# Kernel tuning notes

Hardware: AMD Instinct MI355X
Metric: run time of the kernel (lower is better)

Reference implementation:

```python
import jax, jax.numpy as jnp
import numpy as np

# ---- constants lifted from EulerRNNCell / run_model ----
OMEGA_EPS = 1e-8          # inputs + 1e-08
GAMMA = 1.1               # self.params[1]
ETA = 0.36                # self.params[2]
DT = 2.0 ** (-8)          # deltat
MAXT = 1.0
NUM_TRAJ = 64
T = int(np.arange(0.0, MAXT, DT).shape[0])   # 256 time points
B = 512


def setup_inputs() -> dict:
    key = jax.random.key(0)
    k1, k2 = jax.random.split(key)
    inputs = jax.random.normal(k1, (B, 1), dtype=jnp.float32)      # per-sample Rabi rate Omega
    # rho0 = |0><0|  ->  Bloch vector (0, 0, 1)
    bloch0 = jnp.zeros((3,), dtype=jnp.float32).at[2].set(1.0)
    # unit normals; Euler-Maruyama scaling sqrt(DT) applied inside reference
    wvec = jax.random.normal(k2, (NUM_TRAJ * B, T - 1, 2), dtype=jnp.float32)
    return {"inputs": inputs, "bloch0": bloch0, "wvec": wvec}


def _euler_rollout(x0, omega, dw):
    """Sequential Euler-Maruyama rollout of the Genois qubit SDE.
    x0:    [N, 3]       initial Bloch vectors
    omega: [N]          per-trajectory Rabi rate (params[:,0])
    dw:    [T-1, N, 2]  Wiener increments (already scaled by sqrt(DT))
    returns x_T: [N, 3]
    """
    k = jnp.asarray(np.sqrt(GAMMA * ETA / 2.0), dtype=x0.dtype)  # measurement back-action strength

    def step(x, dwt):
        x1, x2, x3 = x[:, 0], x[:, 1], x[:, 2]
        # drift a(x, p): Rabi drive about x-axis + measurement dephasing at GAMMA/2
        ax = -0.5 * GAMMA * x1
        ay = -omega * x3 - 0.5 * GAMMA * x2
        az = omega * x2
        # diffusion b(x, p) @ dW: heterodyne sigma_z back-action (two quadratures)
        d1, d2 = dwt[:, 0], dwt[:, 1]
        bx = k * (-x1 * x3 * d1 + x2 * d2)
        by = k * (-x2 * x3 * d1 - x1 * d2)
        bz = k * ((1.0 - x3 * x3) * d1)
        xn = jnp.stack([x1 + DT * ax + bx,
                        x2 + DT * ay + by,
                        x3 + DT * az + bz], axis=1)
        return xn, None

    xT, _ = jax.lax.scan(step, x0, dw)
    return xT


def reference(inputs, bloch0, wvec):
    b = inputs.shape[0]
    n = NUM_TRAJ * b
    # traj_inputs = tile([inputs+eps, Gamma, eta], num_traj); only Omega varies per row
    omega = jnp.tile(inputs[:, 0] + OMEGA_EPS, (NUM_TRAJ,))          # [N]
    x0 = jnp.broadcast_to(bloch0[None, :], (n, 3)).astype(inputs.dtype)
    dw = jnp.transpose(wvec, (1, 0, 2)) * np.float32(np.sqrt(DT))    # [T-1, N, 2]
    xT = _euler_rollout(x0, omega, dw)                               # [N, 3]
    # reduce_mean over the num_traj replicas (linear, so mean of Bloch == Bloch of mean rho)
    xm = xT.reshape(NUM_TRAJ, b, 3).mean(axis=0)                     # [B, 3]
    px = 0.5 * (xm[:, 0] + 1.0)
    py = 0.5 * (xm[:, 1] + 1.0)
    pz = 0.5 * (xm[:, 2] + 1.0)
    probs = jnp.stack([px, 1.0 - px, py, 1.0 - py, pz, 1.0 - pz], axis=1)
    probs = jnp.clip(probs, 0.0, 1.0)
    out = jnp.concatenate([probs, inputs], axis=1)                   # [B, 7]
    # new recurrent state: flattened rho = (I + x.sigma)/2 at final time
    rho = jnp.stack([(1.0 + xm[:, 2]) * 0.5,
                     (xm[:, 0] - 1j * xm[:, 1]) * 0.5,
                     (xm[:, 0] + 1j * xm[:, 1]) * 0.5,
                     (1.0 - xm[:, 2]) * 0.5], axis=1).astype(jnp.complex64)
    return out, rho
```

## Files before the change

kernel.cpp:

```cpp
#include <hip/hip_runtime.h>


#define BATCH   512
#define NTRAJ   64
#define TSTEPS  255

__device__ __forceinline__ void sde_step(float& x1, float& x2, float& x3,
                                         float w1, float w2, float omega)
{
    const float HG = 0.55f;
    const float K  = 0.44497190922573976f;
    const float SD = 0.0625f;
    const float DT = 0.00390625f;

    const float d1 = w1 * SD;
    const float d2 = w2 * SD;

    const float ax = -HG * x1;
    const float ay = -omega * x3 - HG * x2;
    const float az = omega * x2;

    const float bx = K * (-x1 * x3 * d1 + x2 * d2);
    const float by = K * (-x2 * x3 * d1 - x1 * d2);
    const float bz = K * ((1.0f - x3 * x3) * d1);

    const float y1 = x1 + DT * ax + bx;
    const float y2 = x2 + DT * ay + by;
    const float y3 = x3 + DT * az + bz;
    x1 = y1; x2 = y2; x3 = y3;
}

__device__ __forceinline__ void sde_step2(float& x1, float& x2, float& x3,
                                          float4 w, float omega)
{
    sde_step(x1, x2, x3, w.x, w.y, omega);
    sde_step(x1, x2, x3, w.z, w.w, omega);
}

__global__ __launch_bounds__(64) void euler_rollout_kernel(
    const float* __restrict__ inputs,
    const float* __restrict__ bloch0,
    const float* __restrict__ wvec,
    float* __restrict__ out,
    int out_size)
{
    const int b = blockIdx.x;
    const int j = threadIdx.x;
    const long long n = (long long)j * BATCH + b;

    const float omega = inputs[b] + 1e-8f;

    float x1 = bloch0[0];
    float x2 = bloch0[1];
    float x3 = bloch0[2];

    const float2* __restrict__ wrow =
        reinterpret_cast<const float2*>(wvec) + n * TSTEPS;

    const int head = (b & 1);
    if (head) {
        const float2 wh = wrow[0];
        sde_step(x1, x2, x3, wh.x, wh.y, omega);
    }
    const float4* __restrict__ w4 =
        reinterpret_cast<const float4*>(wrow + head);

    float4 a0, a1, a2, a3, c0, c1, c2, c3;
    a0 = w4[0]; a1 = w4[1]; a2 = w4[2]; a3 = w4[3];

    int k = 0;
#pragma unroll 1
    for (int it = 0; it < 15; ++it) {
        c0 = w4[k + 4]; c1 = w4[k + 5]; c2 = w4[k + 6]; c3 = w4[k + 7];
        sde_step2(x1, x2, x3, a0, omega);
        sde_step2(x1, x2, x3, a1, omega);
        sde_step2(x1, x2, x3, a2, omega);
        sde_step2(x1, x2, x3, a3, omega);
        a0 = w4[k + 8]; a1 = w4[k + 9]; a2 = w4[k + 10]; a3 = w4[k + 11];
        sde_step2(x1, x2, x3, c0, omega);
        sde_step2(x1, x2, x3, c1, omega);
        sde_step2(x1, x2, x3, c2, omega);
        sde_step2(x1, x2, x3, c3, omega);
        k += 8;
    }
    sde_step2(x1, x2, x3, a0, omega);
    sde_step2(x1, x2, x3, a1, omega);
    sde_step2(x1, x2, x3, a2, omega);
    sde_step2(x1, x2, x3, a3, omega);
    c0 = w4[124]; c1 = w4[125]; c2 = w4[126];
    sde_step2(x1, x2, x3, c0, omega);
    sde_step2(x1, x2, x3, c1, omega);
    sde_step2(x1, x2, x3, c2, omega);
    if (!head) {
        const float2 wt = wrow[254];
        sde_step(x1, x2, x3, wt.x, wt.y, omega);
    }

#pragma unroll
    for (int off = 32; off > 0; off >>= 1) {
        x1 += __shfl_xor(x1, off);
        x2 += __shfl_xor(x2, off);
        x3 += __shfl_xor(x3, off);
    }

    if (j == 0) {
        const float inv = 1.0f / (float)NTRAJ;
        const float xm1 = x1 * inv;
        const float xm2 = x2 * inv;
        const float xm3 = x3 * inv;

        float px = 0.5f * (xm1 + 1.0f);
        float py = 0.5f * (xm2 + 1.0f);
        float pz = 0.5f * (xm3 + 1.0f);

        float p0 = fminf(fmaxf(px, 0.0f), 1.0f);
        float p1 = fminf(fmaxf(1.0f - px, 0.0f), 1.0f);
        float p2 = fminf(fmaxf(py, 0.0f), 1.0f);
        float p3 = fminf(fmaxf(1.0f - py, 0.0f), 1.0f);
        float p4 = fminf(fmaxf(pz, 0.0f), 1.0f);
        float p5 = fminf(fmaxf(1.0f - pz, 0.0f), 1.0f);

        float* o = out + (long long)b * 7;
        o[0] = p0; o[1] = p1; o[2] = p2; o[3] = p3; o[4] = p4; o[5] = p5;
        o[6] = inputs[b];

        float* rre = out + BATCH * 7 + (long long)b * 4;
        rre[0] = (1.0f + xm3) * 0.5f;
        rre[1] = xm1 * 0.5f;
        rre[2] = xm1 * 0.5f;
        rre[3] = (1.0f - xm3) * 0.5f;

        if (out_size >= BATCH * 7 + BATCH * 8) {
            float* rim = out + BATCH * 7 + BATCH * 4 + (long long)b * 4;
            rim[0] = 0.0f;
            rim[1] = -xm2 * 0.5f;
            rim[2] = xm2 * 0.5f;
            rim[3] = 0.0f;
        }
    }
}

extern "C" void kernel_launch(void* const* d_in, const int* in_sizes, int n_in,
                              void* d_out, int out_size, void* d_ws, size_t ws_size,
                              hipStream_t stream) {
    const float* inputs = (const float*)d_in[0];
    const float* bloch0 = (const float*)d_in[1];
    const float* wvec   = (const float*)d_in[2];
    float* out = (float*)d_out;

    euler_rollout_kernel<<<dim3(BATCH), dim3(64), 0, stream>>>(
        inputs, bloch0, wvec, out, out_size);
}
```

Measured before the change: 106.8 us.

## Remap trajectories to contiguous threads and split reduction into a second kernel

After: 113.8 us. 1.07x slower.

```diff
diff --git a/kernel.cpp b/kernel.cpp
--- a/kernel.cpp
+++ b/kernel.cpp
@@ -3,6 +3,7 @@
 
 #define BATCH   512
 #define NTRAJ   64
+#define NTOT    (BATCH * NTRAJ)
 #define TSTEPS  255
 
 __device__ __forceinline__ void sde_step(float& x1, float& x2, float& x3,
@@ -41,12 +42,10 @@
     const float* __restrict__ inputs,
     const float* __restrict__ bloch0,
     const float* __restrict__ wvec,
-    float* __restrict__ out,
-    int out_size)
+    float* __restrict__ xs)
 {
-    const int b = blockIdx.x;
-    const int j = threadIdx.x;
-    const long long n = (long long)j * BATCH + b;
+    const int n = blockIdx.x * 64 + threadIdx.x;
+    const int b = n & (BATCH - 1);
 
     const float omega = inputs[b] + 1e-8f;
 
@@ -55,9 +54,9 @@
     float x3 = bloch0[2];
 
     const float2* __restrict__ wrow =
-        reinterpret_cast<const float2*>(wvec) + n * TSTEPS;
+        reinterpret_cast<const float2*>(wvec) + (long long)n * TSTEPS;
 
-    const int head = (b & 1);
+    const int head = (n & 1);
     if (head) {
         const float2 wh = wrow[0];
         sde_step(x1, x2, x3, wh.x, wh.y, omega);
@@ -96,47 +95,60 @@
         sde_step(x1, x2, x3, wt.x, wt.y, omega);
     }
 
-#pragma unroll
-    for (int off = 32; off > 0; off >>= 1) {
-        x1 += __shfl_xor(x1, off);
-        x2 += __shfl_xor(x2, off);
-        x3 += __shfl_xor(x3, off);
+    xs[n]            = x1;
+    xs[NTOT + n]     = x2;
+    xs[2 * NTOT + n] = x3;
+}
+
+__global__ __launch_bounds__(64) void reduce_epilogue_kernel(
+    const float* __restrict__ inputs,
+    const float* __restrict__ xs,
+    float* __restrict__ out,
+    int out_size)
+{
+    const int b = blockIdx.x * 64 + threadIdx.x;
+
+    float s1 = 0.0f, s2 = 0.0f, s3 = 0.0f;
+#pragma unroll 8
+    for (int r = 0; r < NTRAJ; ++r) {
+        const int n = r * BATCH + b;
+        s1 += xs[n];
+        s2 += xs[NTOT + n];
+        s3 += xs[2 * NTOT + n];
     }
 
-    if (j == 0) {
-        const float inv = 1.0f / (float)NTRAJ;
-        const float xm1 = x1 * inv;
-        const float xm2 = x2 * inv;
-        const float xm3 = x3 * inv;
+    const float inv = 1.0f / (float)NTRAJ;
+    const float xm1 = s1 * inv;
+    const float xm2 = s2 * inv;
+    const float xm3 = s3 * inv;
 
-        float px = 0.5f * (xm1 + 1.0f);
-        float py = 0.5f * (xm2 + 1.0f);
-        float pz = 0.5f * (xm3 + 1.0f);
+    float px = 0.5f * (xm1 + 1.0f);
+    float py = 0.5f * (xm2 + 1.0f);
+    float pz = 0.5f * (xm3 + 1.0f);
 
-        float p0 = fminf(fmaxf(px, 0.0f), 1.0f);
-        float p1 = fminf(fmaxf(1.0f - px, 0.0f), 1.0f);
-        float p2 = fminf(fmaxf(py, 0.0f), 1.0f);
-        float p3 = fminf(fmaxf(1.0f - py, 0.0f), 1.0f);
-        float p4 = fminf(fmaxf(pz, 0.0f), 1.0f);
-        float p5 = fminf(fmaxf(1.0f - pz, 0.0f), 1.0f);
+    float p0 = fminf(fmaxf(px, 0.0f), 1.0f);
+    float p1 = fminf(fmaxf(1.0f - px, 0.0f), 1.0f);
+    float p2 = fminf(fmaxf(py, 0.0f), 1.0f);
+    float p3 = fminf(fmaxf(1.0f - py, 0.0f), 1.0f);
+    float p4 = fminf(fmaxf(pz, 0.0f), 1.0f);
+    float p5 = fminf(fmaxf(1.0f - pz, 0.0f), 1.0f);
 
-        float* o = out + (long long)b * 7;
-        o[0] = p0; o[1] = p1; o[2] = p2; o[3] = p3; o[4] = p4; o[5] = p5;
-        o[6] = inputs[b];
+    float* o = out + (long long)b * 7;
+    o[0] = p0; o[1] = p1; o[2] = p2; o[3] = p3; o[4] = p4; o[5] = p5;
+    o[6] = inputs[b];
 
-        float* rre = out + BATCH * 7 + (long long)b * 4;
-        rre[0] = (1.0f + xm3) * 0.5f;
-        rre[1] = xm1 * 0.5f;
-        rre[2] = xm1 * 0.5f;
-        rre[3] = (1.0f - xm3) * 0.5f;
+    float* rre = out + BATCH * 7 + (long long)b * 4;
+    rre[0] = (1.0f + xm3) * 0.5f;
+    rre[1] = xm1 * 0.5f;
+    rre[2] = xm1 * 0.5f;
+    rre[3] = (1.0f - xm3) * 0.5f;
 
-        if (out_size >= BATCH * 7 + BATCH * 8) {
-            float* rim = out + BATCH * 7 + BATCH * 4 + (long long)b * 4;
-            rim[0] = 0.0f;
-            rim[1] = -xm2 * 0.5f;
-            rim[2] = xm2 * 0.5f;
-            rim[3] = 0.0f;
-        }
+    if (out_size >= BATCH * 7 + BATCH * 8) {
+        float* rim = out + BATCH * 7 + BATCH * 4 + (long long)b * 4;
+        rim[0] = 0.0f;
+        rim[1] = -xm2 * 0.5f;
+        rim[2] = xm2 * 0.5f;
+        rim[3] = 0.0f;
     }
 }
 
@@ -147,7 +159,10 @@
     const float* bloch0 = (const float*)d_in[1];
     const float* wvec   = (const float*)d_in[2];
     float* out = (float*)d_out;
+    float* xs  = (float*)d_ws;
 
-    euler_rollout_kernel<<<dim3(BATCH), dim3(64), 0, stream>>>(
-        inputs, bloch0, wvec, out, out_size);
+    euler_rollout_kernel<<<dim3(NTOT / 64), dim3(64), 0, stream>>>(
+        inputs, bloch0, wvec, xs);
+    reduce_epilogue_kernel<<<dim3(BATCH / 64), dim3(64), 0, stream>>>(
+        inputs, xs, out, out_size);
 }
```
